# Kernel tuning notes

Measured on AMD Instinct MI355X. Metric: run time of the kernel, lower is better.

## Reference

```python
import jax, jax.numpy as jnp
import numpy as np

B, T, C, H = 2, 2048, 1024, 16
D = C // H
EPS = 1e-5

def _layer_norm(x, w, b):
    mu = jnp.mean(x, axis=-1, keepdims=True)
    var = jnp.var(x, axis=-1, keepdims=True)
    return (x - mu) * jax.lax.rsqrt(var + EPS) * w + b

def setup_inputs() -> dict:
    key = jax.random.key(0)
    ks = jax.random.split(key, 8)
    s = 0.02
    return {
        "x": jax.random.normal(ks[0], (B, T, C), jnp.float32),
        "ln1_w": jnp.ones((C,), jnp.float32),
        "ln1_b": jnp.zeros((C,), jnp.float32),
        "wq": jax.random.normal(ks[1], (C, C), jnp.float32) * s,
        "bq": jnp.zeros((C,), jnp.float32),
        "wk": jax.random.normal(ks[2], (C, C), jnp.float32) * s,
        "bk": jnp.zeros((C,), jnp.float32),
        "wv": jax.random.normal(ks[3], (C, C), jnp.float32) * s,
        "bv": jnp.zeros((C,), jnp.float32),
        "wo": jax.random.normal(ks[4], (C, C), jnp.float32) * s,
        "bo": jnp.zeros((C,), jnp.float32),
        "ln2_w": jnp.ones((C,), jnp.float32),
        "ln2_b": jnp.zeros((C,), jnp.float32),
        "w1": jax.random.normal(ks[5], (C, 4 * C), jnp.float32) * s,
        "b1": jnp.zeros((4 * C,), jnp.float32),
        "w2": jax.random.normal(ks[6], (4 * C, C), jnp.float32) * s,
        "b2": jnp.zeros((C,), jnp.float32),
    }

def reference(x, ln1_w, ln1_b, wq, bq, wk, bk, wv, bv, wo, bo,
              ln2_w, ln2_b, w1, b1, w2, b2):
    # --- attention branch ---
    h = _layer_norm(x, ln1_w, ln1_b)
    q = (h @ wq + bq).reshape(B, T, H, D).transpose(0, 2, 1, 3)  # [B,H,T,D]
    k = (h @ wk + bk).reshape(B, T, H, D).transpose(0, 2, 1, 3)
    v = (h @ wv + bv).reshape(B, T, H, D).transpose(0, 2, 1, 3)
    att = jnp.einsum("bhqd,bhkd->bhqk", q, k) * (1.0 / np.sqrt(D))
    causal = jnp.tril(jnp.ones((T, T), dtype=bool))
    att = jnp.where(causal[None, None], att, jnp.float32(-jnp.inf))
    att = jax.nn.softmax(att, axis=-1)
    y = jnp.einsum("bhqk,bhkd->bhqd", att, v)
    y = y.transpose(0, 2, 1, 3).reshape(B, T, C)
    y = y @ wo + bo
    x = x + y
    # --- MLP branch ---
    h = _layer_norm(x, ln2_w, ln2_b)
    h = jax.nn.gelu(h @ w1 + b1, approximate=False)
    h = h @ w2 + b2
    return x + h
```

## Files before the change

### kernel.cpp

```cpp
#include <hip/hip_runtime.h>
#include <hip/hip_bf16.h>
#include <math.h>

#define B_  2
#define T_  2048
#define C_  1024
#define H_  16
#define D_  64
#define BT_ (B_*T_)

typedef __hip_bfloat16 bf16;
typedef short bf16x8 __attribute__((ext_vector_type(8)));
typedef float floatx4 __attribute__((ext_vector_type(4)));

struct alignas(8) bf4 { bf16 v[4]; };

#define GLOAD_LDS16(g, l) __builtin_amdgcn_global_load_lds(            \
    (const __attribute__((address_space(1))) void*)(g),                \
    (__attribute__((address_space(3))) void*)(l), 16, 0, 0)

__device__ __forceinline__ void ln_body(const float* __restrict__ x,
    const float* __restrict__ w, const float* __restrict__ b,
    bf16* __restrict__ out, const int row)
{
    __shared__ float ps[4], ps2[4];
    __shared__ float sm, srs;
    const int tid = threadIdx.x;
    float4 v = ((const float4*)(x + (size_t)row * C_))[tid];
    float s  = v.x + v.y + v.z + v.w;
    float s2 = v.x*v.x + v.y*v.y + v.z*v.z + v.w*v.w;
    for (int off = 32; off > 0; off >>= 1) {
        s  += __shfl_down(s,  off);
        s2 += __shfl_down(s2, off);
    }
    const int wid = tid >> 6;
    if ((tid & 63) == 0) { ps[wid] = s; ps2[wid] = s2; }
    __syncthreads();
    if (tid == 0) {
        float ts  = ps[0] + ps[1] + ps[2] + ps[3];
        float ts2 = ps2[0] + ps2[1] + ps2[2] + ps2[3];
        float mean = ts * (1.0f / C_);
        float var  = ts2 * (1.0f / C_) - mean * mean;
        sm  = mean;
        srs = rsqrtf(var + 1e-5f);
    }
    __syncthreads();
    const float mean = sm, rs = srs;
    float4 wv = ((const float4*)w)[tid];
    float4 bv = ((const float4*)b)[tid];
    bf4 o;
    o.v[0] = __float2bfloat16((v.x - mean) * rs * wv.x + bv.x);
    o.v[1] = __float2bfloat16((v.y - mean) * rs * wv.y + bv.y);
    o.v[2] = __float2bfloat16((v.z - mean) * rs * wv.z + bv.z);
    o.v[3] = __float2bfloat16((v.w - mean) * rs * wv.w + bv.w);
    *(bf4*)(out + (size_t)row * C_ + tid * 4) = o;
}

__global__ __launch_bounds__(256) void ln_bf16_kernel(const float* __restrict__ x,
    const float* __restrict__ w, const float* __restrict__ b,
    bf16* __restrict__ out)
{
    ln_body(x, w, b, out, blockIdx.x);
}

__device__ __forceinline__ void wconv_body(const float* __restrict__ W,
    bf16* __restrict__ Wt, int K, int N, int k0, int n0)
{
    __shared__ float L[64][65];
    const int t = threadIdx.x;
    const int r = t >> 4, c4 = t & 15;
    #pragma unroll
    for (int p = 0; p < 4; ++p) {
        const int kr = p * 16 + r;
        const float4 v = *(const float4*)(W + (size_t)(k0 + kr) * N + n0 + c4 * 4);
        L[kr][c4*4+0] = v.x; L[kr][c4*4+1] = v.y;
        L[kr][c4*4+2] = v.z; L[kr][c4*4+3] = v.w;
    }
    __syncthreads();
    #pragma unroll
    for (int p = 0; p < 4; ++p) {
        const int nr = p * 16 + r;
        bf4 o;
        o.v[0] = __float2bfloat16(L[c4*4+0][nr]);
        o.v[1] = __float2bfloat16(L[c4*4+1][nr]);
        o.v[2] = __float2bfloat16(L[c4*4+2][nr]);
        o.v[3] = __float2bfloat16(L[c4*4+3][nr]);
        *(bf4*)(Wt + (size_t)(n0 + nr) * K + k0 + c4 * 4) = o;
    }
}

__global__ __launch_bounds__(256) void prep_kernel(
    const float* __restrict__ x, const float* __restrict__ ln1_w,
    const float* __restrict__ ln1_b,
    const float* __restrict__ wq, const float* __restrict__ wk,
    const float* __restrict__ wv, const float* __restrict__ wo,
    const float* __restrict__ bq, const float* __restrict__ bk,
    const float* __restrict__ bv,
    const float* __restrict__ w1, const float* __restrict__ w2,
    bf16* __restrict__ h, bf16* __restrict__ wqkvT, bf16* __restrict__ woT,
    bf16* __restrict__ w1T, bf16* __restrict__ w2T,
    float* __restrict__ bqkv)
{
    const int b = blockIdx.x;
    if (b < 1024) {
        const int z = b >> 8, rem = b & 255;
        const float* W = (z == 0) ? wq : (z == 1) ? wk : (z == 2) ? wv : wo;
        bf16* Wt = (z == 3) ? woT : wqkvT + (size_t)z * 1024 * 1024;
        wconv_body(W, Wt, 1024, 1024, (rem & 15) * 64, (rem >> 4) * 64);
    } else if (b < 3072) {
        const int c = b - 1024, z = c >> 10, r = c & 1023;
        if (z == 0) wconv_body(w1, w1T, 1024, 4096, (r & 15) * 64, (r >> 4) * 64);
        else        wconv_body(w2, w2T, 4096, 1024, (r >> 4) * 64, (r & 15) * 64);
    } else if (b < 7168) {
        ln_body(x, ln1_w, ln1_b, h, b - 3072);
    } else {
        const int i = (b - 7168) * 256 + threadIdx.x;
        float v = (i < 1024) ? bq[i] : (i < 2048 ? bk[i - 1024] : bv[i - 2048]);
        bqkv[i] = v;
    }
}

__global__ __launch_bounds__(256) void splitk2_kernel(
    float* __restrict__ out, const float* __restrict__ p1)
{
    const size_t i = (size_t)blockIdx.x * 256 + threadIdx.x;
    float4 o = ((const float4*)out)[i];
    const float4 p = ((const float4*)p1)[i];
    o.x += p.x; o.y += p.y; o.z += p.z; o.w += p.w;
    ((float4*)out)[i] = o;
}

template<int TM, int TN, int BK>
__global__ __launch_bounds__(256) void mfma_gemm_t(
    const bf16* __restrict__ A, const bf16* __restrict__ Wt,
    const float* __restrict__ bias, const float* __restrict__ res,
    void* __restrict__ outv, bf16* __restrict__ vT, float* __restrict__ psplit,
    int M, int N, int K, int ldk, int mode)
{
    constexpr int MI = TM / 32;
    constexpr int NJ = TN / 32;
    constexpr int CPR = BK / 8;
    constexpr int NSLOT = (TM + TN) * CPR / 256;
    __shared__ __align__(16) bf16 smem[(TM + TN) * BK];
    bf16* As = smem;
    bf16* Bs = smem + TM * BK;
    const int tid = threadIdx.x;
    const int w = tid >> 6, l = tid & 63;
    const int fm = l & 15, qd = l >> 4;
    const int m0 = blockIdx.x * TM, n0 = blockIdx.y * TN;
    const int bz = blockIdx.z;
    const int wr = (w >> 1) * (TM / 2), wc = (w & 1) * (TN / 2);

    const bf16* Ab = A  + (size_t)bz * K;
    const bf16* Wb = Wt + (size_t)bz * K;

    const bf16* gsrc[NSLOT];
    bf16* ldst[NSLOT];
    #pragma unroll
    for (int p = 0; p < NSLOT; ++p) {
        const int s = tid + p * 256;
        if (s < TM * CPR) {
            const int row = s / CPR, pos = s % CPR;
            const int ch = pos ^ (row & (CPR - 1));
            gsrc[p] = Ab + (size_t)(m0 + row) * ldk + ch * 8;
            ldst[p] = As + s * 8;
        } else {
            const int s2 = s - TM * CPR;
            const int row = s2 / CPR, pos = s2 % CPR;
            const int ch = pos ^ (row & (CPR - 1));
            gsrc[p] = Wb + (size_t)(n0 + row) * ldk + ch * 8;
            ldst[p] = Bs + s2 * 8;
        }
    }

    floatx4 acc[MI][NJ] = {};

    const int nk = K / BK;
    for (int kk = 0; kk < nk; ++kk) {
        const size_t ko = (size_t)kk * BK;
        __syncthreads();
        #pragma unroll
        for (int p = 0; p < NSLOT; ++p)
            GLOAD_LDS16(gsrc[p] + ko, ldst[p]);
        __syncthreads();
        #pragma unroll
        for (int ks = 0; ks < BK / 32; ++ks) {
            bf16x8 af[MI], bfr[NJ];
            #pragma unroll
            for (int i = 0; i < MI; ++i) {
                const int row = wr + i * 16 + fm;
                af[i] = *(const bf16x8*)(As + row * BK
                        + (((ks * 4 + qd) ^ (row & (CPR - 1))) * 8));
            }
            #pragma unroll
            for (int j = 0; j < NJ; ++j) {
                const int row = wc + j * 16 + fm;
                bfr[j] = *(const bf16x8*)(Bs + row * BK
                        + (((ks * 4 + qd) ^ (row & (CPR - 1))) * 8));
            }
            #pragma unroll
            for (int i = 0; i < MI; ++i)
                #pragma unroll
                for (int j = 0; j < NJ; ++j)
                    acc[i][j] = __builtin_amdgcn_mfma_f32_16x16x32_bf16(
                        af[i], bfr[j], acc[i][j], 0, 0, 0);
        }
    }

    const int col0 = n0 + wc;
    const int row0 = m0 + wr;
    const bool isv = (mode == 3) && (col0 >= 2048);
    const bool bounce = (mode == 0) || (mode == 1) || (mode == 3 && !isv);
    __syncthreads();

    if (bounce) {
        constexpr int RM = TM / 2, RN = TN / 2, CHN = RN / 8;
        bf16* eb = smem + w * (RM * RN);
        #pragma unroll
        for (int j = 0; j < NJ; ++j) {
            const int col = col0 + j * 16 + fm;
            const float bb = bias[col];
            const bool isq = (mode == 3) && (col0 + j * 16 < 1024);
            const int lc = j * 16 + fm;
            #pragma unroll
            for (int i = 0; i < MI; ++i) {
                floatx4 a = acc[i][j];
                #pragma unroll
                for (int r = 0; r < 4; ++r) {
                    float vv = a[r] + bb;
                    if (mode == 1) {
                        float zz = vv * (0.7978845608f + 0.0356774081f * vv * vv);
                        zz = fminf(zz, 15.0f);
                        const float e = __expf(2.0f * zz);
                        vv = vv * (e / (e + 1.0f));
                    }
                    if (isq) vv *= 0.125f;
                    const int lr = i * 16 + qd * 4 + r;
                    const int pch = ((lc >> 3) + 2 * qd) & (CHN - 1);
                    eb[lr * RN + pch * 8 + (lc & 7)] = __float2bfloat16(vv);
                }
            }
        }
        bf16* o = (bf16*)outv;
        #pragma unroll
        for (int c = 0; c < RM * RN / 512; ++c) {
            const int idx = c * 64 + l;
            const int row = idx / CHN;
            const int c8  = idx % CHN;
            const int pch = (c8 + 2 * ((row >> 2) & 3)) & (CHN - 1);
            const bf16x8 vv = *(const bf16x8*)(eb + row * RN + pch * 8);
            *(bf16x8*)(o + (size_t)(row0 + row) * N + col0 + c8 * 8) = vv;
        }
    } else {
        #pragma unroll
        for (int j = 0; j < NJ; ++j) {
            const int col = col0 + j * 16 + fm;
            const float bb = bias[col];
            #pragma unroll
            for (int i = 0; i < MI; ++i) {
                const int row = row0 + i * 16 + qd * 4;
                floatx4 a = acc[i][j];
                if (mode == 4) {
                    if (bz == 0) {
                        float* o = (float*)outv;
                        #pragma unroll
                        for (int r = 0; r < 4; ++r)
                            o[(size_t)(row + r) * N + col] =
                                a[r] + bb + res[(size_t)(row + r) * N + col];
                    } else {
                        #pragma unroll
                        for (int r = 0; r < 4; ++r)
                            psplit[(size_t)(row + r) * N + col] = a[r];
                    }
                } else if (mode == 2) {
                    float* o = (float*)outv;
                    #pragma unroll
                    for (int r = 0; r < 4; ++r)
                        o[(size_t)(row + r) * N + col] =
                            a[r] + bb + res[(size_t)(row + r) * N + col];
                } else {
                    bf4 pv;
                    #pragma unroll
                    for (int r = 0; r < 4; ++r) pv.v[r] = __float2bfloat16(a[r] + bb);
                    *(bf4*)(vT + (size_t)(col - 2048) * M + row) = pv;
                }
            }
        }
    }
}


#define G8_BARRIER() do {                                   \
    __builtin_amdgcn_sched_barrier(0);                      \
    asm volatile("" ::: "memory");                          \
    __builtin_amdgcn_s_barrier();                           \
    asm volatile("" ::: "memory");                          \
    __builtin_amdgcn_sched_barrier(0);                      \
  } while (0)

#define G8_WAIT_LGKM0() do {                                        \
    asm volatile("s_waitcnt lgkmcnt(0)" ::: "memory");              \
    __builtin_amdgcn_sched_barrier(0);                              \
  } while (0)

#define G8_WAIT_VM(n) asm volatile("s_waitcnt vmcnt(" #n ")" ::: "memory")

#define G8_VW2() do { if (st1) G8_WAIT_VM(8); else G8_WAIT_VM(2); } while (0)
#define G8_VW3() do { if (st1) G8_WAIT_VM(8); else G8_WAIT_VM(0); } while (0)
#define G8_VW1() do { if (st2) G8_WAIT_VM(8); else if (st1) G8_WAIT_VM(4); \
                      else G8_WAIT_VM(0); } while (0)

#define G8_PHASE(Aq, Bq, RA, RB, SC, SG, DB, KO, VW)                           \
  do {                                                                         \
    if (RA) {                                                                  \
      const bf16* pa0 = smem + cur * BUF + aof0 + (Aq) * 8192;                 \
      const bf16* pa1 = smem + cur * BUF + aof1 + (Aq) * 8192;                 \
      _Pragma("unroll")                                                        \
      for (int i = 0; i < 4; ++i) {                                            \
        ar[Aq][i][0] = *(const bf16x8*)(pa0 + i * 1024);                       \
        ar[Aq][i][1] = *(const bf16x8*)(pa1 + i * 1024);                       \
      }                                                                        \
    }                                                                          \
    if (RB) {                                                                  \
      const bf16* pb0 = smem + cur * BUF + bof0 + (Bq) * 2048;                 \
      const bf16* pb1 = smem + cur * BUF + bof1 + (Bq) * 2048;                 \
      _Pragma("unroll")                                                        \
      for (int jj = 0; jj < 2; ++jj) {                                         \
        br[jj][0] = *(const bf16x8*)(pb0 + jj * 1024);                         \
        br[jj][1] = *(const bf16x8*)(pb1 + jj * 1024);                         \
      }                                                                        \
    }                                                                          \
    if (SC) {                                                                  \
      GLOAD_LDS16(gsrc[SG] + (KO), smem + (DB) * BUF + lof[SG]);               \
      GLOAD_LDS16(gsrc[SG] + (KO) + (((SG) & 1) ? gdB : gdA),                  \
                  smem + (DB) * BUF + lof[SG] + (((SG) & 1) ? 8192 : 4096));   \
    }                                                                          \
    VW;                                                                        \
    G8_BARRIER();                                                              \
    G8_WAIT_LGKM0();                                                           \
    __builtin_amdgcn_s_setprio(1);                                             \
    _Pragma("unroll")                                                          \
    for (int i = 0; i < 4; ++i)                                                \
      _Pragma("unroll")                                                        \
      for (int jj = 0; jj < 2; ++jj) {                                         \
        acc[(Aq)*4+i][(Bq)*2+jj] = __builtin_amdgcn_mfma_f32_16x16x32_bf16(    \
            ar[Aq][i][0], br[jj][0], acc[(Aq)*4+i][(Bq)*2+jj], 0, 0, 0);       \
        acc[(Aq)*4+i][(Bq)*2+jj] = __builtin_amdgcn_mfma_f32_16x16x32_bf16(    \
            ar[Aq][i][1], br[jj][1], acc[(Aq)*4+i][(Bq)*2+jj], 0, 0, 0);       \
      }                                                                        \
    __builtin_amdgcn_s_setprio(0);                                             \
  } while (0)

template<int MODE>
__global__ __launch_bounds__(512, 2) void gemm8_t(
    const bf16* __restrict__ A, const bf16* __restrict__ Wt,
    const float* __restrict__ bias, bf16* __restrict__ out,
    bf16* __restrict__ vT, int M, int N, int K)
{
    constexpr int BUF = 32768;
    __shared__ __align__(16) bf16 smem[2 * BUF];

    const int tid = threadIdx.x;
    const int w = tid >> 6, l = tid & 63;
    const int fm = l & 15, qd = l >> 4;
    const int wm = w >> 2, wn = w & 3;

    const int nbx = gridDim.x;
    const int nwg = nbx * gridDim.y;
    const int bid = blockIdx.y * nbx + blockIdx.x;
    const int cpx = nwg >> 3;
    const int swz = (bid & 7) * cpx + (bid >> 3);
    const int m0 = (swz % nbx) * 256;
    const int n0 = (swz / nbx) * 256;

    const size_t gdA = (size_t)64 * K;
    const size_t gdB = (size_t)128 * K;
    const bf16* gsrc[4];
    int lof[4];
    #pragma unroll
    for (int g = 0; g < 4; ++g) {
        const int isB  = (g & 1);
        const int half = (g >> 1);
        const int pos = tid & 7;
        int row, lofe;
        const bf16* gb;
        if (!isB) {
            row  = half * 128 + (tid >> 3);
            gb   = A + (size_t)(m0 + row) * K;
            lofe = row * 64 + pos * 8;
        } else {
            const int vr = tid >> 3;
            row  = (vr >> 5) * 64 + half * 32 + (vr & 31);
            gb   = Wt + (size_t)(n0 + row) * K;
            lofe = 16384 + row * 64 + pos * 8;
        }
        const int ch = pos ^ (row & 7);
        gsrc[g] = gb + ch * 8;
        lof[g]  = lofe;
    }

    const int sw0 = qd ^ (fm & 7);
    const int aof0 = (wm * 64 + fm) * 64 + sw0 * 8;
    const int aof1 = (wm * 64 + fm) * 64 + (sw0 ^ 4) * 8;
    const int bof0 = 16384 + (wn * 64 + fm) * 64 + sw0 * 8;
    const int bof1 = 16384 + (wn * 64 + fm) * 64 + (sw0 ^ 4) * 8;

    floatx4 acc[8][4] = {};
    bf16x8 ar[2][4][2];
    bf16x8 br[2][2];

    GLOAD_LDS16(gsrc[0],       smem + lof[0]);
    GLOAD_LDS16(gsrc[0] + gdA, smem + lof[0] + 4096);
    GLOAD_LDS16(gsrc[1],       smem + lof[1]);
    GLOAD_LDS16(gsrc[1] + gdB, smem + lof[1] + 8192);
    GLOAD_LDS16(gsrc[2],       smem + lof[2]);
    GLOAD_LDS16(gsrc[2] + gdA, smem + lof[2] + 4096);
    GLOAD_LDS16(gsrc[3],       smem + lof[3]);
    GLOAD_LDS16(gsrc[3] + gdB, smem + lof[3] + 8192);
    GLOAD_LDS16(gsrc[1] + 64,       smem + BUF + lof[1]);
    GLOAD_LDS16(gsrc[1] + 64 + gdB, smem + BUF + lof[1] + 8192);
    GLOAD_LDS16(gsrc[0] + 64,       smem + BUF + lof[0]);
    GLOAD_LDS16(gsrc[0] + 64 + gdA, smem + BUF + lof[0] + 4096);
    G8_WAIT_VM(8);
    G8_BARRIER();

    const int nt = K / 64;
    int cur = 0;
    for (int t = 0; t < nt; ++t, cur ^= 1) {
        const bool st1 = (t + 1 < nt);
        const bool st2 = (t + 2 < nt);
        const int nb = cur ^ 1;
        const size_t ko1 = (size_t)(t + 1) * 64;
        const size_t ko2 = (size_t)(t + 2) * 64;
        G8_PHASE(0, 0, 1, 1, st1, 2, nb,  ko1, G8_VW2());
        G8_PHASE(1, 0, 1, 0, st1, 3, nb,  ko1, G8_VW3());
        G8_PHASE(0, 1, 0, 1, st2, 1, cur, ko2, ;);
        G8_PHASE(1, 1, 0, 0, st2, 0, cur, ko2, G8_VW1());
    }

    G8_WAIT_VM(0);
    G8_BARRIER();

    const int colb = n0 + wn * 64;
    if (MODE == 3 && colb >= 2048) {
        #pragma unroll
        for (int jf = 0; jf < 4; ++jf) {
            const int col = colb + jf * 16 + fm;
            const float bb = bias[col];
            #pragma unroll
            for (int f = 0; f < 8; ++f) {
                const int row = m0 + (f >> 2) * 128 + wm * 64 + (f & 3) * 16 + qd * 4;
                bf4 pv;
                #pragma unroll
                for (int r = 0; r < 4; ++r)
                    pv.v[r] = __float2bfloat16(acc[f][jf][r] + bb);
                *(bf4*)(vT + (size_t)(col - 2048) * M + row) = pv;
            }
        }
    } else {
        const float scale = (MODE == 3 && colb < 1024) ? 0.125f : 1.0f;
        bf16* eb = smem + w * 8192;
        #pragma unroll
        for (int jf = 0; jf < 4; ++jf) {
            const int col = colb + jf * 16 + fm;
            const float bb = bias[col];
            const int lc = jf * 16 + fm;
            const int pch = ((lc >> 3) + 2 * qd) & 7;
            #pragma unroll
            for (int f = 0; f < 8; ++f) {
                const int lr = (f & 3) * 16 + qd * 4;
                #pragma unroll
                for (int r = 0; r < 4; ++r) {
                    float vv = acc[f][jf][r] + bb;
                    if (MODE == 1) {
                        float zz = vv * (0.7978845608f + 0.0356774081f * vv * vv);
                        zz = fminf(zz, 15.0f);
                        const float e = __expf(2.0f * zz);
                        vv = vv * (e / (e + 1.0f));
                    }
                    vv *= scale;
                    eb[(f >> 2) * 4096 + (lr + r) * 64 + pch * 8 + (lc & 7)] =
                        __float2bfloat16(vv);
                }
            }
        }
        #pragma unroll
        for (int p = 0; p < 2; ++p)
            #pragma unroll
            for (int c = 0; c < 8; ++c) {
                const int idx = c * 64 + l;
                const int row = idx >> 3, c8 = idx & 7;
                const int pch = (c8 + 2 * ((row >> 2) & 3)) & 7;
                const bf16x8 vv = *(const bf16x8*)(eb + p * 4096 + row * 64 + pch * 8);
                const int rowg = m0 + p * 128 + wm * 64 + row;
                *(bf16x8*)(out + (size_t)rowg * N + colb + c8 * 8) = vv;
            }
    }
}

__global__ __launch_bounds__(256) void attn_mfma_kernel(
    const bf16* __restrict__ qkv, const bf16* __restrict__ vT,
    bf16* __restrict__ y)
{
    const int pi = blockIdx.x, h = blockIdx.y, b = blockIdx.z;
    const int tid = threadIdx.x, w = tid >> 6, l = tid & 63;
    const int fm = l & 15, qd = l >> 4;
    const int qta = pi, qtb = 31 - pi;
    const float M0 = 3.0f;

    __shared__ __align__(16) bf16 Ks[4096];
    __shared__ __align__(16) bf16 Vs[4096];
    __shared__ __align__(16) bf16 Ps[8][1152];

    const int r0 = tid >> 2,         c0 = (tid & 3) ^ ((r0 >> 1) & 3);
    const int r1 = (tid + 256) >> 2, c1 = ((tid + 256) & 3) ^ ((r1 >> 1) & 3);
    const bf16* kbase = qkv + (size_t)(b * T_) * 3072 + 1024 + h * 64;
    const bf16* vbase = vT + (size_t)(h * 64) * BT_ + b * T_;
    const bf16* kg0 = kbase + (size_t)(r0 & 63) * 3072 + (r0 >> 6) * 32 + c0 * 8;
    const bf16* kg1 = kbase + (size_t)(r1 & 63) * 3072 + (r1 >> 6) * 32 + c1 * 8;
    const bf16* vg0 = vbase + (size_t)(r0 & 63) * BT_ + (r0 >> 6) * 32 + c0 * 8;
    const bf16* vg1 = vbase + (size_t)(r1 & 63) * BT_ + (r1 >> 6) * 32 + c1 * 8;
    bf16* ksl0 = Ks + (size_t)(w * 64) * 8;
    bf16* ksl1 = Ks + (size_t)(w * 64 + 256) * 8;
    bf16* vsl0 = Vs + (size_t)(w * 64) * 8;
    bf16* vsl1 = Vs + (size_t)(w * 64 + 256) * 8;

    const bf16* qpa = qkv + (size_t)(b * T_ + qta * 64 + w * 16 + fm) * 3072 + h * 64 + qd * 8;
    const bf16* qpb = qkv + (size_t)(b * T_ + qtb * 64 + w * 16 + fm) * 3072 + h * 64 + qd * 8;
    const bf16x8 qa0 = *(const bf16x8*)qpa, qa1 = *(const bf16x8*)(qpa + 32);
    const bf16x8 qb0 = *(const bf16x8*)qpb, qb1 = *(const bf16x8*)(qpb + 32);

    const int qba = qta * 64 + w * 16 + qd * 4;
    const int qbb = qtb * 64 + w * 16 + qd * 4;
    const int sw = (qd ^ ((fm >> 1) & 3)) * 8;

    float la[4] = {}, lb[4] = {};
    floatx4 Oa[4] = {}, Ob[4] = {};
    bf16* psa = &Ps[w * 2][0];
    bf16* psb = &Ps[w * 2 + 1][0];

    auto tile = [&](const bf16x8 q0, const bf16x8 q1, float* lsum,
                    floatx4* O, bf16* ps, const int kt, const int qt, const int qb) {
        floatx4 S[4];
        #pragma unroll
        for (int nt = 0; nt < 4; ++nt) {
            const int rr = nt * 16 + fm;
            const bf16x8 k0 = *(const bf16x8*)(Ks + rr * 32 + sw);
            const bf16x8 k1 = *(const bf16x8*)(Ks + (64 + rr) * 32 + sw);
            floatx4 s = {};
            s = __builtin_amdgcn_mfma_f32_16x16x32_bf16(q0, k0, s, 0, 0, 0);
            s = __builtin_amdgcn_mfma_f32_16x16x32_bf16(q1, k1, s, 0, 0, 0);
            S[nt] = s;
        }
        if (kt == qt) {
            #pragma unroll
            for (int nt = 0; nt < 4; ++nt) {
                const int key = kt * 64 + nt * 16 + fm;
                #pragma unroll
                for (int r = 0; r < 4; ++r)
                    if (key > qb + r) S[nt][r] = -1e30f;
            }
        }
        #pragma unroll
        for (int nt = 0; nt < 4; ++nt)
            #pragma unroll
            for (int r = 0; r < 4; ++r) {
                const float p = __expf(S[nt][r] - M0);
                lsum[r] += p;
                ps[(qd * 4 + r) * 72 + nt * 16 + fm] = __float2bfloat16(p);
            }
        #pragma unroll
        for (int s2 = 0; s2 < 2; ++s2) {
            const bf16x8 pf = *(const bf16x8*)(ps + fm * 72 + s2 * 32 + qd * 8);
            #pragma unroll
            for (int nt = 0; nt < 4; ++nt) {
                const bf16x8 vf =
                    *(const bf16x8*)(Vs + (s2 * 64 + nt * 16 + fm) * 32 + sw);
                O[nt] = __builtin_amdgcn_mfma_f32_16x16x32_bf16(pf, vf, O[nt], 0, 0, 0);
            }
        }
    };

    for (int kt = 0; kt <= qtb; ++kt) {
        const size_t kOff = (size_t)kt * 64 * 3072;
        const size_t vOff = (size_t)kt * 64;
        __syncthreads();
        GLOAD_LDS16(kg0 + kOff, ksl0);
        GLOAD_LDS16(kg1 + kOff, ksl1);
        GLOAD_LDS16(vg0 + vOff, vsl0);
        GLOAD_LDS16(vg1 + vOff, vsl1);
        __syncthreads();
        tile(qb0, qb1, lb, Ob, psb, kt, qtb, qbb);
        if (kt <= qta)
            tile(qa0, qa1, la, Oa, psa, kt, qta, qba);
    }

    #pragma unroll
    for (int mk = 1; mk < 16; mk <<= 1)
        #pragma unroll
        for (int r = 0; r < 4; ++r) {
            la[r] += __shfl_xor(la[r], mk);
            lb[r] += __shfl_xor(lb[r], mk);
        }

    #pragma unroll
    for (int r = 0; r < 4; ++r) {
        const float inva = 1.0f / la[r];
        const float invb = 1.0f / lb[r];
        const size_t rowa = (size_t)(b * T_) + qba + r;
        const size_t rowb = (size_t)(b * T_) + qbb + r;
        #pragma unroll
        for (int nt = 0; nt < 4; ++nt) {
            y[rowa * C_ + h * 64 + nt * 16 + fm] = __float2bfloat16(Oa[nt][r] * inva);
            y[rowb * C_ + h * 64 + nt * 16 + fm] = __float2bfloat16(Ob[nt][r] * invb);
        }
    }
}

extern "C" void kernel_launch(void* const* d_in, const int* in_sizes, int n_in,
                              void* d_out, int out_size, void* d_ws, size_t ws_size,
                              hipStream_t stream)
{
    const float* x     = (const float*)d_in[0];
    const float* ln1_w = (const float*)d_in[1];
    const float* ln1_b = (const float*)d_in[2];
    const float* wq    = (const float*)d_in[3];
    const float* bq    = (const float*)d_in[4];
    const float* wk    = (const float*)d_in[5];
    const float* bk    = (const float*)d_in[6];
    const float* wv    = (const float*)d_in[7];
    const float* bv    = (const float*)d_in[8];
    const float* wo    = (const float*)d_in[9];
    const float* bo    = (const float*)d_in[10];
    const float* ln2_w = (const float*)d_in[11];
    const float* ln2_b = (const float*)d_in[12];
    const float* w1    = (const float*)d_in[13];
    const float* b1    = (const float*)d_in[14];
    const float* w2    = (const float*)d_in[15];
    const float* b2    = (const float*)d_in[16];
    float* out = (float*)d_out;

    char* ws = (char*)d_ws;
    const size_t MB = 1024 * 1024;
    bf16*  wqkvT = (bf16*)(ws);
    bf16*  woT   = (bf16*)(ws + 6 * MB);
    bf16*  w1T   = (bf16*)(ws + 8 * MB);
    bf16*  w2T   = (bf16*)(ws + 16 * MB);
    float* bqkv  = (float*)(ws + 24 * MB);
    bf16*  h     = (bf16*)(ws + 24 * MB + 65536);
    bf16*  qkv   = (bf16*)(ws + 32 * MB + 65536);
    bf16*  vT    = (bf16*)(ws + 56 * MB + 65536);
    bf16*  y     = (bf16*)(ws + 64 * MB + 65536);
    float* x2    = (float*)(ws + 72 * MB + 65536);
    bf16*  u     = qkv;
    float* p1    = (float*)ws;

    prep_kernel<<<7180, 256, 0, stream>>>(
        x, ln1_w, ln1_b, wq, wk, wv, wo, bq, bk, bv, w1, w2,
        h, wqkvT, woT, w1T, w2T, bqkv);

    gemm8_t<3><<<dim3(16, 12), 512, 0, stream>>>(
        h, wqkvT, bqkv, qkv, vT, BT_, 3072, C_);
    attn_mfma_kernel<<<dim3(16, H_, B_), 256, 0, stream>>>(qkv, vT, y);
    mfma_gemm_t<128, 64, 64><<<dim3(32, 16), 256, 0, stream>>>(
        y, woT, bo, x, x2, nullptr, nullptr, BT_, C_, C_, C_, 2);

    ln_bf16_kernel<<<BT_, 256, 0, stream>>>(x2, ln2_w, ln2_b, h);
    gemm8_t<1><<<dim3(16, 16), 512, 0, stream>>>(
        h, w1T, b1, u, nullptr, BT_, 4 * C_, C_);
    mfma_gemm_t<128, 128, 64><<<dim3(32, 8, 2), 256, 0, stream>>>(
        u, w2T, b2, x2, out, nullptr, p1, BT_, C_, 2 * C_, 4 * C_, 4);
    splitk2_kernel<<<BT_ * C_ / 1024, 256, 0, stream>>>(out, p1);
}
```

Before: 348.4 us.

## Double-buffer K/V tiles in attention kernel with async prefetch

Splits the K and V shared-memory tiles into two buffers so the attention loop can issue global-to-LDS loads for the next key tile before computing on the current one. Explicit vmcnt waits and barriers replace the two syncthreads around each load. The goal is to hide global load latency behind the MFMA work. It doubles the K/V LDS footprint, which may lower occupancy, and it relies on G8_WAIT_VM and G8_BARRIER macros defined elsewhere in the file.

```diff
diff --git a/kernel.cpp b/kernel.cpp
--- a/kernel.cpp
+++ b/kernel.cpp
@@ -508,8 +508,8 @@
     const int qta = pi, qtb = 31 - pi;
     const float M0 = 3.0f;
 
-    __shared__ __align__(16) bf16 Ks[4096];
-    __shared__ __align__(16) bf16 Vs[4096];
+    __shared__ __align__(16) bf16 Ks[2][4096];
+    __shared__ __align__(16) bf16 Vs[2][4096];
     __shared__ __align__(16) bf16 Ps[8][1152];
 
     const int r0 = tid >> 2,         c0 = (tid & 3) ^ ((r0 >> 1) & 3);
@@ -520,15 +520,20 @@
     const bf16* kg1 = kbase + (size_t)(r1 & 63) * 3072 + (r1 >> 6) * 32 + c1 * 8;
     const bf16* vg0 = vbase + (size_t)(r0 & 63) * BT_ + (r0 >> 6) * 32 + c0 * 8;
     const bf16* vg1 = vbase + (size_t)(r1 & 63) * BT_ + (r1 >> 6) * 32 + c1 * 8;
-    bf16* ksl0 = Ks + (size_t)(w * 64) * 8;
-    bf16* ksl1 = Ks + (size_t)(w * 64 + 256) * 8;
-    bf16* vsl0 = Vs + (size_t)(w * 64) * 8;
-    bf16* vsl1 = Vs + (size_t)(w * 64 + 256) * 8;
+    const int kofs0 = (w * 64) * 8;
+    const int kofs1 = (w * 64 + 256) * 8;
 
     const bf16* qpa = qkv + (size_t)(b * T_ + qta * 64 + w * 16 + fm) * 3072 + h * 64 + qd * 8;
     const bf16* qpb = qkv + (size_t)(b * T_ + qtb * 64 + w * 16 + fm) * 3072 + h * 64 + qd * 8;
     const bf16x8 qa0 = *(const bf16x8*)qpa, qa1 = *(const bf16x8*)(qpa + 32);
     const bf16x8 qb0 = *(const bf16x8*)qpb, qb1 = *(const bf16x8*)(qpb + 32);
+    G8_WAIT_VM(0);
+    __builtin_amdgcn_sched_barrier(0);
+
+    GLOAD_LDS16(kg0, &Ks[0][0] + kofs0);
+    GLOAD_LDS16(kg1, &Ks[0][0] + kofs1);
+    GLOAD_LDS16(vg0, &Vs[0][0] + kofs0);
+    GLOAD_LDS16(vg1, &Vs[0][0] + kofs1);
 
     const int qba = qta * 64 + w * 16 + qd * 4;
     const int qbb = qtb * 64 + w * 16 + qd * 4;
@@ -539,14 +544,15 @@
     bf16* psa = &Ps[w * 2][0];
     bf16* psb = &Ps[w * 2 + 1][0];
 
-    auto tile = [&](const bf16x8 q0, const bf16x8 q1, float* lsum,
+    auto tile = [&](const bf16* KsB, const bf16* VsB,
+                    const bf16x8 q0, const bf16x8 q1, float* lsum,
                     floatx4* O, bf16* ps, const int kt, const int qt, const int qb) {
         floatx4 S[4];
         #pragma unroll
         for (int nt = 0; nt < 4; ++nt) {
             const int rr = nt * 16 + fm;
-            const bf16x8 k0 = *(const bf16x8*)(Ks + rr * 32 + sw);
-            const bf16x8 k1 = *(const bf16x8*)(Ks + (64 + rr) * 32 + sw);
+            const bf16x8 k0 = *(const bf16x8*)(KsB + rr * 32 + sw);
+            const bf16x8 k1 = *(const bf16x8*)(KsB + (64 + rr) * 32 + sw);
             floatx4 s = {};
             s = __builtin_amdgcn_mfma_f32_16x16x32_bf16(q0, k0, s, 0, 0, 0);
             s = __builtin_amdgcn_mfma_f32_16x16x32_bf16(q1, k1, s, 0, 0, 0);
@@ -575,24 +581,30 @@
             #pragma unroll
             for (int nt = 0; nt < 4; ++nt) {
                 const bf16x8 vf =
-                    *(const bf16x8*)(Vs + (s2 * 64 + nt * 16 + fm) * 32 + sw);
+                    *(const bf16x8*)(VsB + (s2 * 64 + nt * 16 + fm) * 32 + sw);
                 O[nt] = __builtin_amdgcn_mfma_f32_16x16x32_bf16(pf, vf, O[nt], 0, 0, 0);
             }
         }
     };
 
     for (int kt = 0; kt <= qtb; ++kt) {
-        const size_t kOff = (size_t)kt * 64 * 3072;
-        const size_t vOff = (size_t)kt * 64;
-        __syncthreads();
-        GLOAD_LDS16(kg0 + kOff, ksl0);
-        GLOAD_LDS16(kg1 + kOff, ksl1);
-        GLOAD_LDS16(vg0 + vOff, vsl0);
-        GLOAD_LDS16(vg1 + vOff, vsl1);
-        __syncthreads();
-        tile(qb0, qb1, lb, Ob, psb, kt, qtb, qbb);
+        const int cb = kt & 1, nb = cb ^ 1;
+        G8_BARRIER();
+        if (kt < qtb) {
+            const size_t kOff = (size_t)(kt + 1) * 64 * 3072;
+            const size_t vOff = (size_t)(kt + 1) * 64;
+            GLOAD_LDS16(kg0 + kOff, &Ks[nb][0] + kofs0);
+            GLOAD_LDS16(kg1 + kOff, &Ks[nb][0] + kofs1);
+            GLOAD_LDS16(vg0 + vOff, &Vs[nb][0] + kofs0);
+            GLOAD_LDS16(vg1 + vOff, &Vs[nb][0] + kofs1);
+            G8_WAIT_VM(4);
+        } else {
+            G8_WAIT_VM(0);
+        }
+        G8_BARRIER();
+        tile(&Ks[cb][0], &Vs[cb][0], qb0, qb1, lb, Ob, psb, kt, qtb, qbb);
         if (kt <= qta)
-            tile(qa0, qa1, la, Oa, psa, kt, qta, qba);
+            tile(&Ks[cb][0], &Vs[cb][0], qa0, qa1, la, Oa, psa, kt, qta, qba);
     }
 
     #pragma unroll
```

Result: no change. 344.7 us (-1.1%).
